# Optimization experiments

Hardware: AMD Instinct MI355X
Metric: run time of the kernel (lower is better)

The kernel has to match this reference:

```python
import jax, jax.numpy as jnp
import numpy as np
from jax.ops import segment_sum

N_NODES = 100000
N_EDGES = 1600000
HIDDEN = 128


def gcn_conv(x, src, dst, w, W, b, num_nodes):
    """PyG GCNConv: add self-loops (weight 1), symmetric deg^-1/2 normalization,
    gather from src, scatter-add to dst. x: [N, Fin], W: [Fin, Fout]."""
    loop = jnp.arange(num_nodes, dtype=src.dtype)
    s = jnp.concatenate([src, loop])
    d = jnp.concatenate([dst, loop])
    ww = jnp.concatenate([w, jnp.ones((num_nodes,), dtype=w.dtype)])
    deg = segment_sum(ww, d, num_segments=num_nodes)           # [N]
    dis = jnp.where(deg > 0, jax.lax.rsqrt(jnp.where(deg > 0, deg, 1.0)), 0.0)
    norm = dis[s] * ww * dis[d]                                # [E+N]
    h = x @ W                                                  # [N, Fout]
    msg = norm[:, None] * h[s]                                 # [E+N, Fout]
    out = segment_sum(msg, d, num_segments=num_nodes)          # [N, Fout]
    return out + b


def setup_inputs() -> dict:
    key = jax.random.key(0)
    ks = jax.random.split(key, 12)
    h = HIDDEN
    sc = lambda fan_in: 1.0 / np.sqrt(fan_in)
    return {
        "x": jax.random.normal(ks[0], (N_NODES, 1), dtype=jnp.float32),
        "edge_index": jax.random.randint(ks[1], (2, N_EDGES), 0, N_NODES, dtype=jnp.int64),
        "edge_weight": jax.random.uniform(ks[2], (N_EDGES,), dtype=jnp.float32),
        "W1": jax.random.normal(ks[3], (1, h), dtype=jnp.float32) * sc(1),
        "b1": jnp.zeros((h,), dtype=jnp.float32),
        "W2": jax.random.normal(ks[4], (h, 2 * h), dtype=jnp.float32) * sc(h),
        "b2": jnp.zeros((2 * h,), dtype=jnp.float32),
        "Wl1": jax.random.normal(ks[5], (2 * h, h), dtype=jnp.float32) * sc(2 * h),
        "bl1": jnp.zeros((h,), dtype=jnp.float32),
        "Wl2": jax.random.normal(ks[6], (h, 1), dtype=jnp.float32) * sc(h),
        "bl2": jnp.zeros((1,), dtype=jnp.float32),
    }


def reference(x, edge_index, edge_weight, W1, b1, W2, b2, Wl1, bl1, Wl2, bl2):
    n = x.shape[0]
    src, dst = edge_index[0], edge_index[1]
    h = jax.nn.relu(gcn_conv(x, src, dst, edge_weight, W1, b1, n))
    h = jax.nn.relu(gcn_conv(h, src, dst, edge_weight, W2, b2, n))
    h = jax.nn.relu(h @ Wl1 + bl1)
    return h @ Wl2 + bl2
```

## Files before the change

kernel.cpp:

```cpp
#include <hip/hip_runtime.h>


#define HD 128
#define HD2 256
#define BSHIFT 8
#define BNODES 256
#define SRCBITS 17
#define EPB 4096

typedef __attribute__((ext_vector_type(8))) short bf8_t;
typedef __attribute__((ext_vector_type(4))) float f32x4;

static inline size_t align256(size_t x) { return (x + 255) & ~(size_t)255; }

__device__ inline ushort f2bf(float f) {
    uint u = __float_as_uint(f);
    uint r = u + 0x7fffu + ((u >> 16) & 1u);
    return (ushort)(r >> 16);
}
__device__ inline uint packbf(float a, float b) {
    return (uint)f2bf(a) | ((uint)f2bf(b) << 16);
}

__global__ void k_init(const float* __restrict__ W2, const float* __restrict__ Wl1,
                       ushort* __restrict__ Bt1, ushort* __restrict__ Bt2,
                       int* __restrict__ bfill) {
    int o = blockIdx.x * blockDim.x + threadIdx.x;
    if (o < 512) bfill[o] = 0;
    if (o >= 32768) return;
    {
        int k0 = o & 7, n = (o >> 3) & 255, k8 = o >> 11;
        Bt1[o] = f2bf(W2[(size_t)(k8 * 8 + k0) * 256 + n]);
    }
    {
        int k0 = o & 7, n = (o >> 3) & 127, k8 = o >> 10;
        Bt2[o] = f2bf(Wl1[(size_t)(k8 * 8 + k0) * 128 + n]);
    }
}

__global__ __launch_bounds__(256) void k_part(const int* __restrict__ ei,
                                              const float* __restrict__ ew,
                                              int* __restrict__ bfill,
                                              uint2* __restrict__ stg,
                                              int E, int nbuck, int cap) {
    __shared__ int lcnt[4][512];
    __shared__ int lbase[4][512];
    __shared__ int lpre[512];
    __shared__ int delta[512];
    __shared__ uint2 sstage[EPB];
    __shared__ uint  ga[EPB];
    __shared__ int wscan[8];
    __shared__ int nvs;
    int tid = threadIdx.x;
    int wvid = tid >> 6, lane = tid & 63;
    for (int i = tid; i < 512; i += 256) {
        lcnt[0][i] = 0; lcnt[1][i] = 0; lcnt[2][i] = 0; lcnt[3][i] = 0;
    }
    __syncthreads();
    bool is64 = (ei[1] == 0) && (ei[3] == 0) && (ei[5] == 0) && (ei[7] == 0);
    int e0 = blockIdx.x * EPB;
    uint pack[16]; uint wb[16]; short bkt[16]; short rank[16];
    for (int u = 0; u < 16; u++) {
        int e = e0 + u * 256 + tid;
        bkt[u] = -1;
        if (e < E) {
            int s, d;
            if (is64) { s = ei[2 * e]; d = ei[2 * (E + e)]; }
            else      { s = ei[e];     d = ei[E + e]; }
            bkt[u] = (short)(d >> BSHIFT);
            pack[u] = ((uint)(d & (BNODES - 1)) << SRCBITS) | (uint)s;
            wb[u] = __float_as_uint(ew[e]);
            rank[u] = (short)atomicAdd(&lcnt[wvid][bkt[u]], 1);
        }
    }
    __syncthreads();
    for (int i = tid; i < 512; i += 256) {
        int t0 = lcnt[0][i], t1 = lcnt[1][i], t2 = lcnt[2][i], t3 = lcnt[3][i];
        lbase[0][i] = 0; lbase[1][i] = t0;
        lbase[2][i] = t0 + t1; lbase[3][i] = t0 + t1 + t2;
        lcnt[0][i] = t0 + t1 + t2 + t3;
    }
    __syncthreads();
    int inc[2];
    for (int r = 0; r < 2; r++) {
        int v = lcnt[0][r * 256 + tid];
        for (int off = 1; off < 64; off <<= 1) {
            int u = __shfl_up(v, off);
            if (lane >= off) v += u;
        }
        inc[r] = v;
        if (lane == 63) wscan[r * 4 + wvid] = v;
    }
    __syncthreads();
    if (tid == 0) {
        int run = 0;
        for (int s2 = 0; s2 < 8; s2++) { int t = wscan[s2]; wscan[s2] = run; run += t; }
        nvs = run;
    }
    __syncthreads();
    for (int r = 0; r < 2; r++) {
        int i = r * 256 + tid;
        int tot = lcnt[0][i];
        int excl = inc[r] - tot + wscan[r * 4 + wvid];
        int gb = 0;
        if (tot && i < nbuck) gb = atomicAdd(&bfill[i], tot);
        lpre[i] = excl;
        delta[i] = i * cap + gb - excl;
    }
    __syncthreads();
    for (int u = 0; u < 16; u++)
        if (bkt[u] >= 0) {
            int b = bkt[u];
            int loc = lpre[b] + lbase[wvid][b] + rank[u];
            sstage[loc] = make_uint2(pack[u], wb[u]);
            ga[loc] = (uint)(delta[b] + loc);
        }
    __syncthreads();
    int nv = nvs;
    for (int ch = 0; ch < 16; ch++) {
        int loc = ch * 256 + tid;
        if (loc < nv) stg[ga[loc]] = sstage[loc];
    }
}

__global__ __launch_bounds__(512) void k_fine(const uint2* __restrict__ stg,
                                              const int* __restrict__ bfill,
                                              const float* __restrict__ x,
                                              float* __restrict__ dis,
                                              float* __restrict__ p,
                                              int* __restrict__ rowptr,
                                              int2* __restrict__ cv,
                                              int cap, int N, int E, int nbuck) {
    __shared__ int cnt_l[BNODES];
    __shared__ int base_l[BNODES];
    __shared__ float degf[BNODES];
    __shared__ int wsum[8];
    int b = blockIdx.x, tid = threadIdx.x;
    int lane = tid & 63, wvid = tid >> 6;
    int a = (tid < b && tid < nbuck) ? bfill[tid] : 0;
    for (int off = 32; off > 0; off >>= 1) a += __shfl_xor(a, off);
    if (lane == 0) wsum[wvid] = a;
    __syncthreads();
    int cb = wsum[0] + wsum[1] + wsum[2] + wsum[3] +
             wsum[4] + wsum[5] + wsum[6] + wsum[7];
    int n = bfill[b];
    if (b == nbuck - 1 && tid == 0) rowptr[N] = E;
    const uint2* s = stg + (size_t)b * cap;
    if (tid < BNODES) { cnt_l[tid] = 0; degf[tid] = 1.0f; }
    __syncthreads();
    for (int i = tid; i < n; i += 512)
        atomicAdd(&cnt_l[s[i].x >> SRCBITS], 1);
    __syncthreads();
    int c = 0;
    if (tid < BNODES) { c = cnt_l[tid]; cnt_l[tid] = 0; }
    int v = c;
    for (int off = 1; off < 64; off <<= 1) {
        int u = __shfl_up(v, off);
        if (lane >= off) v += u;
    }
    if (wvid < 4 && lane == 63) wsum[wvid] = v;
    __syncthreads();
    if (tid < BNODES) {
        int wpre = 0;
        for (int k = 0; k < wvid; k++) wpre += wsum[k];
        base_l[tid] = v + wpre - c;
    }
    __syncthreads();
    for (int i = tid; i < n; i += 512) {
        uint2 r = s[i];
        int dl = r.x >> SRCBITS;
        int src = (int)(r.x & ((1u << SRCBITS) - 1));
        int pos = cb + base_l[dl] + atomicAdd(&cnt_l[dl], 1);
        cv[pos] = make_int2(src, (int)r.y);
        atomicAdd(&degf[dl], __uint_as_float(r.y));
    }
    __syncthreads();
    int gid = (b << BSHIFT) + tid;
    if (tid < BNODES && gid < N) {
        rowptr[gid] = cb + base_l[tid];
        float r = rsqrtf(degf[tid]);
        dis[gid] = r;
        p[gid] = r * x[gid];
    }
}

__global__ __launch_bounds__(256) void k_q(const int* __restrict__ rowptr,
                                           const int2* __restrict__ cv,
                                           const float* __restrict__ dis,
                                           const float* __restrict__ p,
                                           float2* __restrict__ tp, int N) {
    int gid = blockIdx.x * blockDim.x + threadIdx.x;
    int wid = gid >> 4;
    int sl = threadIdx.x & 15;
    if (wid >= N) return;
    int beg = rowptr[wid], end = rowptr[wid + 1];
    float s = 0.0f;
    for (int i = beg + sl; i < end; i += 16) {
        int2 pr = cv[i];
        s += __int_as_float(pr.y) * p[pr.x];
    }
    s += __shfl_xor(s, 1);
    s += __shfl_xor(s, 2);
    s += __shfl_xor(s, 4);
    s += __shfl_xor(s, 8);
    if (sl == 0) {
        float r = dis[wid];
        tp[wid] = make_float2(r * (s + p[wid]), r);
    }
}

__global__ __launch_bounds__(256) void k_agg(const int* __restrict__ rowptr,
                                             const int2* __restrict__ cv,
                                             const float2* __restrict__ tp,
                                             const float* __restrict__ W1,
                                             const float* __restrict__ b1,
                                             uint* __restrict__ z, int N) {
    __shared__ float2 eb[4][64];
    int tid = threadIdx.x;
    int wvid = tid >> 6, lane = tid & 63;
    int half = lane >> 5, hl = lane & 31;
    int node = ((blockIdx.x * 256 + tid) >> 6) * 2 + half;
    bool valid = node < N;
    float4 w1 = valid ? *(const float4*)(W1 + hl * 4) : make_float4(0, 0, 0, 0);
    float4 bb = valid ? *(const float4*)(b1 + hl * 4) : make_float4(0, 0, 0, 0);
    int beg = 0, end = 0;
    if (valid) { beg = rowptr[node]; end = rowptr[node + 1]; }
    int nb = (end - beg + 31) >> 5;
    nb = max(nb, __shfl_xor(nb, 32));
    float4 aA = make_float4(0, 0, 0, 0), aB = make_float4(0, 0, 0, 0);
    const float4* ebp = (const float4*)&eb[wvid][half * 32];
    for (int bt = 0; bt < nb; bt++) {
        int eidx = beg + bt * 32 + hl;
        float wd = 0.0f, tt = 0.0f;
        if (eidx < end) {
            int2 pr = cv[eidx];
            float2 tps = tp[pr.x];
            wd = __int_as_float(pr.y) * tps.y;
            tt = tps.x;
        }
        eb[wvid][lane] = make_float2(wd, tt);
        int m = min(32, end - (beg + bt * 32)); if (m < 0) m = 0;
        int hm = (m + 1) >> 1;
        hm = max(hm, __shfl_xor(hm, 32));
        int u = 0;
        for (; u + 2 <= hm; u += 2) {
            float4 e2 = ebp[u];
            float4 e3 = ebp[u + 1];
            aA.x = fmaf(e2.x, fmaxf(fmaf(e2.y, w1.x, bb.x), 0.f), aA.x);
            aA.y = fmaf(e2.x, fmaxf(fmaf(e2.y, w1.y, bb.y), 0.f), aA.y);
            aA.z = fmaf(e2.x, fmaxf(fmaf(e2.y, w1.z, bb.z), 0.f), aA.z);
            aA.w = fmaf(e2.x, fmaxf(fmaf(e2.y, w1.w, bb.w), 0.f), aA.w);
            aA.x = fmaf(e2.z, fmaxf(fmaf(e2.w, w1.x, bb.x), 0.f), aA.x);
            aA.y = fmaf(e2.z, fmaxf(fmaf(e2.w, w1.y, bb.y), 0.f), aA.y);
            aA.z = fmaf(e2.z, fmaxf(fmaf(e2.w, w1.z, bb.z), 0.f), aA.z);
            aA.w = fmaf(e2.z, fmaxf(fmaf(e2.w, w1.w, bb.w), 0.f), aA.w);
            aB.x = fmaf(e3.x, fmaxf(fmaf(e3.y, w1.x, bb.x), 0.f), aB.x);
            aB.y = fmaf(e3.x, fmaxf(fmaf(e3.y, w1.y, bb.y), 0.f), aB.y);
            aB.z = fmaf(e3.x, fmaxf(fmaf(e3.y, w1.z, bb.z), 0.f), aB.z);
            aB.w = fmaf(e3.x, fmaxf(fmaf(e3.y, w1.w, bb.w), 0.f), aB.w);
            aB.x = fmaf(e3.z, fmaxf(fmaf(e3.w, w1.x, bb.x), 0.f), aB.x);
            aB.y = fmaf(e3.z, fmaxf(fmaf(e3.w, w1.y, bb.y), 0.f), aB.y);
            aB.z = fmaf(e3.z, fmaxf(fmaf(e3.w, w1.z, bb.z), 0.f), aB.z);
            aB.w = fmaf(e3.z, fmaxf(fmaf(e3.w, w1.w, bb.w), 0.f), aB.w);
        }
        if (u < hm) {
            float4 e2 = ebp[u];
            aA.x = fmaf(e2.x, fmaxf(fmaf(e2.y, w1.x, bb.x), 0.f), aA.x);
            aA.y = fmaf(e2.x, fmaxf(fmaf(e2.y, w1.y, bb.y), 0.f), aA.y);
            aA.z = fmaf(e2.x, fmaxf(fmaf(e2.y, w1.z, bb.z), 0.f), aA.z);
            aA.w = fmaf(e2.x, fmaxf(fmaf(e2.y, w1.w, bb.w), 0.f), aA.w);
            aA.x = fmaf(e2.z, fmaxf(fmaf(e2.w, w1.x, bb.x), 0.f), aA.x);
            aA.y = fmaf(e2.z, fmaxf(fmaf(e2.w, w1.y, bb.y), 0.f), aA.y);
            aA.z = fmaf(e2.z, fmaxf(fmaf(e2.w, w1.z, bb.z), 0.f), aA.z);
            aA.w = fmaf(e2.z, fmaxf(fmaf(e2.w, w1.w, bb.w), 0.f), aA.w);
        }
    }
    if (!valid) return;
    float2 tpd = tp[node];
    float rd = tpd.y;
    float o0 = rd * (aA.x + aB.x + rd * fmaxf(fmaf(tpd.x, w1.x, bb.x), 0.f));
    float o1 = rd * (aA.y + aB.y + rd * fmaxf(fmaf(tpd.x, w1.y, bb.y), 0.f));
    float o2 = rd * (aA.z + aB.z + rd * fmaxf(fmaf(tpd.x, w1.z, bb.z), 0.f));
    float o3 = rd * (aA.w + aB.w + rd * fmaxf(fmaf(tpd.x, w1.w, bb.w), 0.f));
    ((uint2*)(z + (size_t)node * 64))[hl] = make_uint2(packbf(o0, o1), packbf(o2, o3));
}

__global__ __launch_bounds__(256) void k_mlp(const ushort* __restrict__ A,
                                             const ushort* __restrict__ Bt1,
                                             const ushort* __restrict__ Bt2,
                                             const float* __restrict__ b2,
                                             const float* __restrict__ bl1,
                                             const float* __restrict__ wl2,
                                             const float* __restrict__ bl2,
                                             float* __restrict__ out, int M) {
    __shared__ ushort st[4][32][40];
    int tid = threadIdx.x;
    int wv = tid >> 6, lane = tid & 63;
    int l15 = lane & 15, quad = lane >> 4;
    int row0 = blockIdx.x * 128 + wv * 32;
    int r0 = row0 + l15;      r0 = r0 < M ? r0 : M - 1;
    int r1 = row0 + 16 + l15; r1 = r1 < M ? r1 : M - 1;

    bf8_t a1[2][4];
    for (int kc = 0; kc < 4; kc++) {
        a1[0][kc] = *(const bf8_t*)(A + (size_t)r0 * 128 + kc * 32 + quad * 8);
        a1[1][kc] = *(const bf8_t*)(A + (size_t)r1 * 128 + kc * 32 + quad * 8);
    }
    f32x4 acc2[2][8];
    for (int i = 0; i < 2; i++)
        for (int j = 0; j < 8; j++) acc2[i][j] = (f32x4){0.f, 0.f, 0.f, 0.f};

    for (int c = 0; c < 8; c++) {
        f32x4 acc1[2][2];
        for (int i = 0; i < 2; i++)
            for (int j = 0; j < 2; j++) acc1[i][j] = (f32x4){0.f, 0.f, 0.f, 0.f};
        for (int kc = 0; kc < 4; kc++)
            for (int nt = 0; nt < 2; nt++) {
                bf8_t b = *(const bf8_t*)(Bt1 +
                    ((size_t)(kc * 4 + quad) * 256 + c * 32 + nt * 16 + l15) * 8);
                acc1[0][nt] = __builtin_amdgcn_mfma_f32_16x16x32_bf16(a1[0][kc], b, acc1[0][nt], 0, 0, 0);
                acc1[1][nt] = __builtin_amdgcn_mfma_f32_16x16x32_bf16(a1[1][kc], b, acc1[1][nt], 0, 0, 0);
            }
        for (int nt = 0; nt < 2; nt++) {
            float bb = b2[c * 32 + nt * 16 + l15];
            for (int mt = 0; mt < 2; mt++)
                for (int rg = 0; rg < 4; rg++)
                    st[wv][mt * 16 + quad * 4 + rg][nt * 16 + l15] =
                        f2bf(fmaxf(acc1[mt][nt][rg] + bb, 0.f));
        }
        bf8_t a2_0 = *(const bf8_t*)&st[wv][l15][quad * 8];
        bf8_t a2_1 = *(const bf8_t*)&st[wv][16 + l15][quad * 8];
        for (int nt2 = 0; nt2 < 8; nt2++) {
            bf8_t b = *(const bf8_t*)(Bt2 +
                ((size_t)(c * 4 + quad) * 128 + nt2 * 16 + l15) * 8);
            acc2[0][nt2] = __builtin_amdgcn_mfma_f32_16x16x32_bf16(a2_0, b, acc2[0][nt2], 0, 0, 0);
            acc2[1][nt2] = __builtin_amdgcn_mfma_f32_16x16x32_bf16(a2_1, b, acc2[1][nt2], 0, 0, 0);
        }
    }
    float rs[2][4] = {};
    for (int nt2 = 0; nt2 < 8; nt2++) {
        int col = nt2 * 16 + l15;
        float bb = bl1[col], ww = wl2[col];
        for (int mt = 0; mt < 2; mt++)
            for (int rg = 0; rg < 4; rg++)
                rs[mt][rg] += fmaxf(acc2[mt][nt2][rg] + bb, 0.f) * ww;
    }
    float base = bl2[0];
    for (int mt = 0; mt < 2; mt++)
        for (int rg = 0; rg < 4; rg++) {
            float s = rs[mt][rg];
            s += __shfl_xor(s, 1);
            s += __shfl_xor(s, 2);
            s += __shfl_xor(s, 4);
            s += __shfl_xor(s, 8);
            int row = row0 + mt * 16 + quad * 4 + rg;
            if (l15 == 0 && row < M) out[row] = s + base;
        }
}

extern "C" void kernel_launch(void* const* d_in, const int* in_sizes, int n_in,
                              void* d_out, int out_size, void* d_ws, size_t ws_size,
                              hipStream_t stream) {
    const float* x   = (const float*)d_in[0];
    const int*   ei  = (const int*)d_in[1];
    const float* ew  = (const float*)d_in[2];
    const float* W1  = (const float*)d_in[3];
    const float* b1  = (const float*)d_in[4];
    const float* W2  = (const float*)d_in[5];
    const float* b2  = (const float*)d_in[6];
    const float* Wl1 = (const float*)d_in[7];
    const float* bl1 = (const float*)d_in[8];
    const float* Wl2 = (const float*)d_in[9];
    const float* bl2 = (const float*)d_in[10];
    float* out = (float*)d_out;
    const int N = in_sizes[0];
    const int E = in_sizes[2];

    const int nbuck = (N + BNODES - 1) >> BSHIFT;
    const int cap = ((((E / nbuck) * 5) / 4 + 1024) + 7) & ~7;

    char* w = (char*)d_ws;
    size_t off = 0;
    auto alloc = [&](size_t bytes) -> void* {
        void* p = w + off;
        off = align256(off + bytes);
        return p;
    };
    uint*   z      = (uint*)alloc((size_t)N * 64 * 4);
    float2* tp     = (float2*)alloc((size_t)N * 8);
    float*  dis    = (float*)alloc((size_t)N * 4);
    float*  p_     = (float*)alloc((size_t)N * 4);
    int*    rowptr = (int*)alloc((size_t)(N + 1) * 4);
    int2*   cv     = (int2*)alloc((size_t)E * 8);
    uint2*  stg    = (uint2*)alloc((size_t)nbuck * cap * 8);
    int*    bfill  = (int*)alloc(512 * 4);
    ushort* Bt1    = (ushort*)alloc(32768 * 2);
    ushort* Bt2    = (ushort*)alloc(32768 * 2);

    k_init<<<128, 256, 0, stream>>>(W2, Wl1, Bt1, Bt2, bfill);
    k_part<<<(E + EPB - 1) / EPB, 256, 0, stream>>>(ei, ew, bfill, stg, E, nbuck, cap);
    k_fine<<<nbuck, 512, 0, stream>>>(stg, bfill, x, dis, p_, rowptr, cv, cap, N, E, nbuck);
    k_q<<<(N * 16 + 255) / 256, 256, 0, stream>>>(rowptr, cv, dis, p_, tp, N);
    k_agg<<<(N + 7) / 8, 256, 0, stream>>>(rowptr, cv, tp, W1, b1, z, N);
    k_mlp<<<(N + 127) / 128, 256, 0, stream>>>((const ushort*)z, Bt1, Bt2,
                                               b2, bl1, Wl2, bl2, out, N);
}
```

Before: 195.6 us.

## Split fine bucket sort into two half-bucket blocks of 256 threads

Each 256-node bucket is now handled by two blocks of 256 threads, each owning half of the destination nodes. Each block still reads the whole bucket twice, filtering to its half, and computes the low-half count to offset its rowptr. The degree accumulation moves into the counting pass, and rowptr/dis/p are written before the scatter pass. This doubles the block count for more parallelism (about 391 buckets is fewer than needed to fill the GPU well) at the cost of redundant reads of the staged edges.

```diff
diff --git a/kernel.cpp b/kernel.cpp
--- a/kernel.cpp
+++ b/kernel.cpp
@@ -123,7 +123,7 @@
     }
 }
 
-__global__ __launch_bounds__(512) void k_fine(const uint2* __restrict__ stg,
+__global__ __launch_bounds__(256) void k_fine(const uint2* __restrict__ stg,
                                               const int* __restrict__ bfill,
                                               const float* __restrict__ x,
                                               float* __restrict__ dis,
@@ -131,56 +131,68 @@
                                               int* __restrict__ rowptr,
                                               int2* __restrict__ cv,
                                               int cap, int N, int E, int nbuck) {
-    __shared__ int cnt_l[BNODES];
-    __shared__ int base_l[BNODES];
-    __shared__ float degf[BNODES];
-    __shared__ int wsum[8];
-    int b = blockIdx.x, tid = threadIdx.x;
+    __shared__ int cnt_l[128];
+    __shared__ int base_l[128];
+    __shared__ float degf[128];
+    __shared__ int wsum[4];
+    __shared__ int wlow[4];
+    __shared__ int ws2[2];
+    int B = blockIdx.x >> 1, h = blockIdx.x & 1;
+    int tid = threadIdx.x;
     int lane = tid & 63, wvid = tid >> 6;
-    int a = (tid < b && tid < nbuck) ? bfill[tid] : 0;
+    int a = (tid < B) ? bfill[tid] : 0;
+    if (tid + 256 < B) a += bfill[tid + 256];
     for (int off = 32; off > 0; off >>= 1) a += __shfl_xor(a, off);
     if (lane == 0) wsum[wvid] = a;
-    __syncthreads();
-    int cb = wsum[0] + wsum[1] + wsum[2] + wsum[3] +
-             wsum[4] + wsum[5] + wsum[6] + wsum[7];
-    int n = bfill[b];
-    if (b == nbuck - 1 && tid == 0) rowptr[N] = E;
-    const uint2* s = stg + (size_t)b * cap;
-    if (tid < BNODES) { cnt_l[tid] = 0; degf[tid] = 1.0f; }
-    __syncthreads();
-    for (int i = tid; i < n; i += 512)
-        atomicAdd(&cnt_l[s[i].x >> SRCBITS], 1);
-    __syncthreads();
-    int c = 0;
-    if (tid < BNODES) { c = cnt_l[tid]; cnt_l[tid] = 0; }
+    if (tid < 128) { cnt_l[tid] = 0; degf[tid] = 1.0f; }
+    __syncthreads();
+    int cb = wsum[0] + wsum[1] + wsum[2] + wsum[3];
+    int n = bfill[B];
+    if (B == nbuck - 1 && h == 0 && tid == 0) rowptr[N] = E;
+    const uint2* s = stg + (size_t)B * cap;
+    int mylow = 0;
+    for (int i = tid; i < n; i += 256) {
+        uint2 r = s[i];
+        int dl = r.x >> SRCBITS;
+        mylow += (dl < 128) ? 1 : 0;
+        if ((dl >> 7) == h) {
+            atomicAdd(&cnt_l[dl & 127], 1);
+            atomicAdd(&degf[dl & 127], __uint_as_float(r.y));
+        }
+    }
+    for (int off = 32; off > 0; off >>= 1) mylow += __shfl_xor(mylow, off);
+    if (lane == 0) wlow[wvid] = mylow;
+    __syncthreads();
+    int lowsum = h ? (wlow[0] + wlow[1] + wlow[2] + wlow[3]) : 0;
+    int c = (tid < 128) ? cnt_l[tid] : 0;
     int v = c;
     for (int off = 1; off < 64; off <<= 1) {
         int u = __shfl_up(v, off);
         if (lane >= off) v += u;
     }
-    if (wvid < 4 && lane == 63) wsum[wvid] = v;
-    __syncthreads();
-    if (tid < BNODES) {
-        int wpre = 0;
-        for (int k = 0; k < wvid; k++) wpre += wsum[k];
+    if (wvid < 2 && lane == 63) ws2[wvid] = v;
+    __syncthreads();
+    if (tid < 128) {
+        int wpre = (wvid == 1) ? ws2[0] : 0;
         base_l[tid] = v + wpre - c;
-    }
-    __syncthreads();
-    for (int i = tid; i < n; i += 512) {
-        uint2 r = s[i];
-        int dl = r.x >> SRCBITS;
-        int src = (int)(r.x & ((1u << SRCBITS) - 1));
-        int pos = cb + base_l[dl] + atomicAdd(&cnt_l[dl], 1);
-        cv[pos] = make_int2(src, (int)r.y);
-        atomicAdd(&degf[dl], __uint_as_float(r.y));
-    }
-    __syncthreads();
-    int gid = (b << BSHIFT) + tid;
-    if (tid < BNODES && gid < N) {
-        rowptr[gid] = cb + base_l[tid];
+        cnt_l[tid] = 0;
+    }
+    __syncthreads();
+    int gid = (B << BSHIFT) + (h << 7) + tid;
+    if (tid < 128 && gid < N) {
+        rowptr[gid] = cb + lowsum + base_l[tid];
         float r = rsqrtf(degf[tid]);
         dis[gid] = r;
         p[gid] = r * x[gid];
+    }
+    for (int i = tid; i < n; i += 256) {
+        uint2 r = s[i];
+        int dl = r.x >> SRCBITS;
+        if ((dl >> 7) == h) {
+            int src = (int)(r.x & ((1u << SRCBITS) - 1));
+            int pos = cb + lowsum + base_l[dl & 127] + atomicAdd(&cnt_l[dl & 127], 1);
+            cv[pos] = make_int2(src, (int)r.y);
+        }
     }
 }
 
@@ -399,7 +411,7 @@
 
     k_init<<<128, 256, 0, stream>>>(W2, Wl1, Bt1, Bt2, bfill);
     k_part<<<(E + EPB - 1) / EPB, 256, 0, stream>>>(ei, ew, bfill, stg, E, nbuck, cap);
-    k_fine<<<nbuck, 512, 0, stream>>>(stg, bfill, x, dis, p_, rowptr, cv, cap, N, E, nbuck);
+    k_fine<<<2 * nbuck, 256, 0, stream>>>(stg, bfill, x, dis, p_, rowptr, cv, cap, N, E, nbuck);
     k_q<<<(N * 16 + 255) / 256, 256, 0, stream>>>(rowptr, cv, dis, p_, tp, N);
     k_agg<<<(N + 7) / 8, 256, 0, stream>>>(rowptr, cv, tp, W1, b1, z, N);
     k_mlp<<<(N + 127) / 128, 256, 0, stream>>>((const ushort*)z, Bt1, Bt2,
```

New measurement: 203.6 us. 1.04x slower.
